# Optimization experiments

Measured on AMD Instinct MI355X. Metric: run time of the kernel, lower is better.

## Reference

```python
import jax, jax.numpy as jnp
import numpy as np
import math

DIM = 1024
NUM_HEADS = 16
QUANTUM_HEADS = 2
HEAD_DIM = DIM // NUM_HEADS          # 64
TRAD_HEADS = NUM_HEADS - QUANTUM_HEADS  # 14
B, S = 1, 1024
STEPS = 2048
LN_EPS = 1e-5


def setup_inputs() -> dict:
    key = jax.random.key(0)
    ks = jax.random.split(key, 10)
    hd2 = 2 * HEAD_DIM
    return {
        "x": jax.random.normal(ks[0], (B, S, DIM), jnp.float32),
        # to_quantum_state: Linear(head_dim -> 2*head_dim) + LayerNorm + Tanh (shared across quantum heads)
        "qs_W": jax.random.normal(ks[1], (hd2, HEAD_DIM), jnp.float32) / math.sqrt(HEAD_DIM),
        "qs_b": jnp.zeros((hd2,), jnp.float32),
        "ln_g": jnp.ones((hd2,), jnp.float32),
        "ln_b": jnp.zeros((hd2,), jnp.float32),
        # per-quantum-head scalars
        "q_freq": jax.random.normal(ks[2], (QUANTUM_HEADS,), jnp.float32) * 0.02,
        "q_shift": jax.random.normal(ks[3], (QUANTUM_HEADS,), jnp.float32) * 0.02,
        # traditional head projections (no bias)
        "Wq": jax.random.normal(ks[4], (TRAD_HEADS * HEAD_DIM, DIM), jnp.float32) / math.sqrt(DIM),
        "Wk": jax.random.normal(ks[5], (TRAD_HEADS * HEAD_DIM, DIM), jnp.float32) / math.sqrt(DIM),
        "Wv": jax.random.normal(ks[6], (TRAD_HEADS * HEAD_DIM, DIM), jnp.float32) / math.sqrt(DIM),
        # output projection (with bias)
        "Wo": jax.random.normal(ks[7], (DIM, DIM), jnp.float32) / math.sqrt(DIM),
        "bo": jnp.zeros((DIM,), jnp.float32),
    }


def _layernorm(h, g, b):
    mu = jnp.mean(h, axis=-1, keepdims=True)
    var = jnp.mean(jnp.square(h - mu), axis=-1, keepdims=True)
    return (h - mu) * jax.lax.rsqrt(var + LN_EPS) * g + b


def _forward(x, qs_W, qs_b, ln_g, ln_b, q_freq, q_shift, Wq, Wk, Wv, Wo, bo):
    cos_table = jnp.cos(jnp.linspace(0.0, 2.0 * math.pi, STEPS).astype(jnp.float32))
    scale = 1.0 / math.sqrt(HEAD_DIM)
    two_pi = 2.0 * math.pi

    outs = []
    # ---- quantum heads (small fixed loop over structurally distinct heads) ----
    for h in range(QUANTUM_HEADS):
        xh = x[..., h * HEAD_DIM:(h + 1) * HEAD_DIM]          # (B,S,hd)
        qs = jnp.tanh(_layernorm(xh @ qs_W.T + qs_b, ln_g, ln_b))  # (B,S,2hd)
        amp, phase = jnp.split(qs, 2, axis=-1)                 # each (B,S,hd)
        # per (query pos i, key pos j, feature d) phase difference
        pd = (phase[:, :, None, :] - phase[:, None, :, :]) * q_freq[h] + q_shift[h]  # (B,S,S,hd)
        idx = jnp.floor(jnp.mod(pd / two_pi * STEPS, STEPS)).astype(jnp.int32)
        interf = cos_table[idx]                                # lookup-table gather, (B,S,S,hd)
        attn = jnp.einsum('bid,bjd,bijd->bij', amp, amp, interf) * scale
        attn = jax.nn.softmax(attn, axis=-1)
        outs.append(attn @ xh)                                 # (B,S,hd), values are the raw head slice

    # ---- traditional heads: standard multi-head attention ----
    q = (x @ Wq.T).reshape(B, S, TRAD_HEADS, HEAD_DIM)
    k = (x @ Wk.T).reshape(B, S, TRAD_HEADS, HEAD_DIM)
    v = (x @ Wv.T).reshape(B, S, TRAD_HEADS, HEAD_DIM)
    scores = jnp.einsum('bqhd,bkhd->bhqk', q, k) * scale       # (B,Ht,S,S)
    probs = jax.nn.softmax(scores, axis=-1)
    trad = jnp.einsum('bhqk,bkhd->bqhd', probs, v).reshape(B, S, TRAD_HEADS * HEAD_DIM)
    outs.append(trad)

    out = jnp.concatenate(outs, axis=-1)                       # (B,S,DIM)
    return out @ Wo.T + bo


def reference(x, qs_W, qs_b, ln_g, ln_b, q_freq, q_shift, Wq, Wk, Wv, Wo, bo):
    return _forward(x, qs_W, qs_b, ln_g, ln_b, q_freq, q_shift, Wq, Wk, Wv, Wo, bo)
```

## Files before the change

kernel.cpp:

```cpp
#include <hip/hip_runtime.h>
#include <hip/hip_bf16.h>
#include <math.h>

#define DIMX 1024
#define SEQ  1024
#define HD   64
#define QH   2
#define TH   14
#define QKVN 2688
#define LN_EPS 1e-5f
#define NB_F2B 4736
#define NB_QPREP 1024
#define NB_XT 32

typedef __bf16 bf16x8 __attribute__((ext_vector_type(8)));
typedef float  f32x4  __attribute__((ext_vector_type(4)));
typedef unsigned short u16x8 __attribute__((ext_vector_type(8)));

__device__ inline unsigned short f2b_rne(float f) {
  unsigned int u = __float_as_uint(f);
  unsigned int r = (u + 0x7FFF + ((u >> 16) & 1)) >> 16;
  return (unsigned short)r;
}

__device__ inline float waveRedSum(float v) {
  #pragma unroll
  for (int off = 32; off; off >>= 1) v += __shfl_xor(v, off, 64);
  return v;
}

__global__ __launch_bounds__(256) void k_prep(
    const float* __restrict__ x, const float* __restrict__ qsW,
    const float* __restrict__ qsb, const float* __restrict__ lng,
    const float* __restrict__ lnb, const float* __restrict__ qfreq,
    const float* __restrict__ qshift,
    const float* __restrict__ wq, const float* __restrict__ wk,
    const float* __restrict__ wv, const float* __restrict__ wo,
    unsigned short* __restrict__ x_bf, unsigned short* __restrict__ wqkv_bf,
    unsigned short* __restrict__ wo_bf,
    unsigned short* __restrict__ qcs, unsigned short* __restrict__ kcs,
    unsigned short* __restrict__ xt) {
  __shared__ float xrow2[2][HD];
  __shared__ float redm[2][2], redv[2][2];
  __shared__ float qsv2[2][128];
  __shared__ unsigned short ttile[64][72];
  int t = threadIdx.x;
  int bid = blockIdx.x;
  if (bid < NB_F2B) {
    long i = ((long)bid * 256 + t) * 4;
    float4 v;
    unsigned short* dst;
    if (i < 1048576) {
      v = *reinterpret_cast<const float4*>(x + i);
      dst = x_bf + i;
    } else if (i < 3801088) {
      long j = i - 1048576;
      const float* s = (j < 917504) ? wq + j
                     : (j < 1835008) ? wk + (j - 917504)
                                     : wv + (j - 1835008);
      v = *reinterpret_cast<const float4*>(s);
      dst = wqkv_bf + j;
    } else {
      long j = i - 3801088;
      v = *reinterpret_cast<const float4*>(wo + j);
      dst = wo_bf + j;
    }
    ushort4 o;
    o.x = f2b_rne(v.x); o.y = f2b_rne(v.y); o.z = f2b_rne(v.z); o.w = f2b_rne(v.w);
    *reinterpret_cast<ushort4*>(dst) = o;
  } else if (bid < NB_F2B + NB_QPREP) {
    int half = t >> 7, o = t & 127;
    int row = (bid - NB_F2B) * 2 + half;
    int h = row >> 10, i = row & 1023;
    if (o < HD) xrow2[half][o] = x[i * DIMX + h * HD + o];
    __syncthreads();
    float s = qsb[o];
    #pragma unroll
    for (int d = 0; d < HD; d += 4) {
      float4 w = *reinterpret_cast<const float4*>(qsW + o * HD + d);
      float4 xv = *reinterpret_cast<const float4*>(&xrow2[half][d]);
      s += xv.x * w.x + xv.y * w.y + xv.z * w.z + xv.w * w.w;
    }
    int wid = (o >> 6), lane = o & 63;
    float ws = waveRedSum(s);
    if (lane == 0) redm[half][wid] = ws;
    __syncthreads();
    float mu = (redm[half][0] + redm[half][1]) * (1.0f / 128.0f);
    float dv = s - mu;
    float ws2 = waveRedSum(dv * dv);
    if (lane == 0) redv[half][wid] = ws2;
    __syncthreads();
    float var = (redv[half][0] + redv[half][1]) * (1.0f / 128.0f);
    float y = dv * rsqrtf(var + LN_EPS) * lng[o] + lnb[o];
    qsv2[half][o] = tanhf(y);
    __syncthreads();
    float freq = qfreq[h], shift = qshift[h];
    size_t base = ((size_t)h * 1024 + i) * 128;
    if (o < HD) {
      float amp = qsv2[half][o];
      float a = qsv2[half][64 + o] * freq + shift;
      float sn, cs;
      __sincosf(a, &sn, &cs);
      qcs[base + o]      = f2b_rne(amp * cs);
      qcs[base + 64 + o] = f2b_rne(amp * sn);
    } else {
      int d = o - 64;
      float amp = qsv2[half][d];
      float bAng = qsv2[half][64 + d] * freq;
      float sn, cs;
      __sincosf(bAng, &sn, &cs);
      kcs[base + d]      = f2b_rne(amp * cs);
      kcs[base + 64 + d] = f2b_rne(amp * sn);
    }
  } else {
    int b = bid - (NB_F2B + NB_QPREP);
    int h = b >> 4, kv0 = (b & 15) * 64;
    #pragma unroll
    for (int pass = 0; pass < 2; ++pass) {
      int s = pass * 256 + t;
      int r = s >> 3, c8 = (s & 7) * 8;
      const float* src = x + (size_t)(kv0 + r) * DIMX + h * 64 + c8;
      float4 a = *reinterpret_cast<const float4*>(src);
      float4 b4 = *reinterpret_cast<const float4*>(src + 4);
      ushort4 o1, o2;
      o1.x = f2b_rne(a.x);  o1.y = f2b_rne(a.y);  o1.z = f2b_rne(a.z);  o1.w = f2b_rne(a.w);
      o2.x = f2b_rne(b4.x); o2.y = f2b_rne(b4.y); o2.z = f2b_rne(b4.z); o2.w = f2b_rne(b4.w);
      *reinterpret_cast<ushort4*>(&ttile[r][c8]) = o1;
      *reinterpret_cast<ushort4*>(&ttile[r][c8 + 4]) = o2;
    }
    __syncthreads();
    #pragma unroll
    for (int pass = 0; pass < 2; ++pass) {
      int s = pass * 256 + t;
      int d = s >> 3, k8 = (s & 7) * 8;
      u16x8 o;
      #pragma unroll
      for (int j = 0; j < 8; ++j) o[j] = ttile[k8 + j][d];
      *reinterpret_cast<u16x8*>(xt + (size_t)h * 65536 + (size_t)d * 1024 + kv0 + k8) = o;
    }
  }
}

template <int DQK, int NT>
__global__ __launch_bounds__(256) void k_fattn2(
    const unsigned short* __restrict__ Qb, long q_hstep, int ldq,
    const unsigned short* __restrict__ Kb, long k_hstep, int ldk,
    const unsigned short* __restrict__ Vtb, long v_hstep, int slot0,
    float* __restrict__ pout, float* __restrict__ pml) {
  const int LQ = DQK + 8;
  const int KREG = DQK / 32;
  __shared__ unsigned short Qs[64 * (DQK + 8)];
  __shared__ unsigned short KV0[64 * (DQK + 8)];
  __shared__ unsigned short KV1[64 * (DQK + 8)];
  __shared__ unsigned short Ps[64 * 72];
  int h = blockIdx.y, q0 = blockIdx.x * 64, split = blockIdx.z;
  int kv0 = split * (NT * 64);
  int slot = slot0 + h * gridDim.z + split;
  int t = threadIdx.x, lane = t & 63, w = t >> 6;
  int g = lane >> 4, li = lane & 15;
  const unsigned short* Qp = Qb + (size_t)h * q_hstep;
  const unsigned short* Kp = Kb + (size_t)h * k_hstep;
  const unsigned short* Vp = Vtb + (size_t)h * v_hstep;

  #pragma unroll
  for (int i = 0; i < DQK / 32; ++i) {
    int s = i * 64 + lane;
    int r = s / (DQK / 8), c8 = (s % (DQK / 8)) * 8;
    u16x8 v = *reinterpret_cast<const u16x8*>(Qp + (size_t)(q0 + w * 16 + r) * ldq + c8);
    *reinterpret_cast<u16x8*>(&Qs[(w * 16 + r) * LQ + c8]) = v;
  }

  u16x8 kreg[KREG], vreg[2];
  auto loadK = [&](int tile) {
    int j0 = kv0 + tile * 64;
    #pragma unroll
    for (int i = 0; i < KREG; ++i) {
      int s = i * 256 + t;
      int r = s / (DQK / 8), c8 = (s % (DQK / 8)) * 8;
      kreg[i] = *reinterpret_cast<const u16x8*>(Kp + (size_t)(j0 + r) * ldk + c8);
    }
  };
  auto writeK = [&](int buf) {
    unsigned short* Kd = buf ? KV1 : KV0;
    #pragma unroll
    for (int i = 0; i < KREG; ++i) {
      int s = i * 256 + t;
      int r = s / (DQK / 8), c8 = (s % (DQK / 8)) * 8;
      *reinterpret_cast<u16x8*>(&Kd[r * LQ + c8]) = kreg[i];
    }
  };
  auto loadV = [&](int tile) {
    int j0 = kv0 + tile * 64;
    #pragma unroll
    for (int i = 0; i < 2; ++i) {
      int s = i * 256 + t;
      int d = s >> 3, c8 = (s & 7) * 8;
      vreg[i] = *reinterpret_cast<const u16x8*>(Vp + (size_t)d * 1024 + j0 + c8);
    }
  };
  auto writeV = [&](int buf) {
    unsigned short* Vd = buf ? KV1 : KV0;
    #pragma unroll
    for (int i = 0; i < 2; ++i) {
      int s = i * 256 + t;
      int d = s >> 3, c8 = (s & 7) * 8;
      *reinterpret_cast<u16x8*>(&Vd[d * 72 + c8]) = vreg[i];
    }
  };

  loadK(0); writeK(0); loadK(1); loadV(0);
  __syncthreads();

  f32x4 s_all[NT][4] = {};

  #pragma unroll
  for (int tile = 0; tile < NT; ++tile) {
    const unsigned short* Ksc = (tile & 1) ? KV1 : KV0;
    if (tile < NT - 1) writeK((tile + 1) & 1);
    if (tile < NT - 2) loadK(tile + 2);
    if (tile == NT - 1) writeV(0);
    #pragma unroll
    for (int kk = 0; kk < DQK / 32; ++kk) {
      bf16x8 aq = *reinterpret_cast<const bf16x8*>(&Qs[(w * 16 + li) * LQ + kk * 32 + g * 8]);
      #pragma unroll
      for (int n = 0; n < 4; ++n) {
        bf16x8 bk = *reinterpret_cast<const bf16x8*>(&Ksc[(n * 16 + li) * LQ + kk * 32 + g * 8]);
        s_all[tile][n] = __builtin_amdgcn_mfma_f32_16x16x32_bf16(aq, bk, s_all[tile][n], 0, 0, 0);
      }
    }
    __syncthreads();
  }

  loadV(1);

  float mrow[4], lrow[4];
  #pragma unroll
  for (int r = 0; r < 4; ++r) {
    float tm = -1e30f;
    #pragma unroll
    for (int tile = 0; tile < NT; ++tile)
      #pragma unroll
      for (int n = 0; n < 4; ++n) tm = fmaxf(tm, s_all[tile][n][r]);
    #pragma unroll
    for (int m = 1; m < 16; m <<= 1) tm = fmaxf(tm, __shfl_xor(tm, m, 64));
    float rs = 0.f;
    #pragma unroll
    for (int tile = 0; tile < NT; ++tile)
      #pragma unroll
      for (int n = 0; n < 4; ++n) {
        float p = __expf((s_all[tile][n][r] - tm) * 0.125f);
        s_all[tile][n][r] = p;
        rs += p;
      }
    #pragma unroll
    for (int m = 1; m < 16; m <<= 1) rs += __shfl_xor(rs, m, 64);
    mrow[r] = tm; lrow[r] = rs;
  }

  f32x4 acc_o[4] = {};
  #pragma unroll
  for (int tile = 0; tile < NT; ++tile) {
    const unsigned short* Vsc = (tile & 1) ? KV1 : KV0;
    if (tile < NT - 1) writeV((tile + 1) & 1);
    if (tile < NT - 2) loadV(tile + 2);
    #pragma unroll
    for (int n = 0; n < 4; ++n)
      #pragma unroll
      for (int r = 0; r < 4; ++r)
        Ps[(w * 16 + g * 4 + r) * 72 + n * 16 + li] = f2b_rne(s_all[tile][n][r]);
    #pragma unroll
    for (int kk = 0; kk < 2; ++kk) {
      bf16x8 ap = *reinterpret_cast<const bf16x8*>(&Ps[(w * 16 + li) * 72 + kk * 32 + g * 8]);
      #pragma unroll
      for (int n = 0; n < 4; ++n) {
        bf16x8 bv = *reinterpret_cast<const bf16x8*>(&Vsc[(n * 16 + li) * 72 + kk * 32 + g * 8]);
        acc_o[n] = __builtin_amdgcn_mfma_f32_16x16x32_bf16(ap, bv, acc_o[n], 0, 0, 0);
      }
    }
    __syncthreads();
  }

  size_t rowbase = (size_t)slot * 1024;
  #pragma unroll
  for (int r = 0; r < 4; ++r) {
    int qr = q0 + w * 16 + g * 4 + r;
    #pragma unroll
    for (int n = 0; n < 4; ++n)
      pout[(rowbase + qr) * 64 + n * 16 + li] = acc_o[n][r];
    if (li == 0) {
      pml[(rowbase + qr) * 2 + 0] = mrow[r];
      pml[(rowbase + qr) * 2 + 1] = lrow[r];
    }
  }
}

__global__ __launch_bounds__(256) void k_fmerge(
    const float* __restrict__ pout, const float* __restrict__ pml,
    unsigned short* __restrict__ concat) {
  int rq = blockIdx.x * 4 + (threadIdx.x >> 6);
  int lh = rq >> 10, q = rq & 1023;
  int d = threadIdx.x & 63;
  int s0 = (lh < 2) ? lh * 8 : 16 + (lh - 2) * 4;
  int ns = (lh < 2) ? 8 : 4;
  float m_s[8], l_s[8];
  float M = -1e30f;
  #pragma unroll
  for (int s = 0; s < 8; ++s) {
    if (s < ns) {
      size_t rb = (size_t)(s0 + s) * 1024 + q;
      m_s[s] = pml[rb * 2 + 0];
      l_s[s] = pml[rb * 2 + 1];
      M = fmaxf(M, m_s[s]);
    }
  }
  float num = 0.f, den = 0.f;
  #pragma unroll
  for (int s = 0; s < 8; ++s) {
    if (s < ns) {
      float wgt = __expf((m_s[s] - M) * 0.125f);
      num += wgt * pout[((size_t)(s0 + s) * 1024 + q) * 64 + d];
      den += wgt * l_s[s];
    }
  }
  concat[(size_t)q * DIMX + lh * 64 + d] = f2b_rne(num / den);
}

template <int HAS_BIAS, int BF16_OUT>
__global__ __launch_bounds__(256) void k_gemm64s(
    const unsigned short* __restrict__ A, const unsigned short* __restrict__ B,
    void* __restrict__ Cv, const float* __restrict__ bias,
    unsigned short* __restrict__ vtp,
    int K, int lda, int ldb, int ldc) {
  __shared__ unsigned short As[64 * 64];
  __shared__ unsigned short Bs[64 * 64];
  int t = threadIdx.x, lane = t & 63, w = t >> 6;
  int wr = w >> 1, wc = w & 1;
  int g = lane >> 4, li = lane & 15;
  int mb = blockIdx.y * 64, nb = blockIdx.x * 64;
  int rstg = t >> 3;
  int cswz = (((t & 7) ^ (rstg & 7)) * 8);
  f32x4 acc[2][2] = {};
  for (int kb = 0; kb < K; kb += 64) {
    __syncthreads();
    #pragma unroll
    for (int i = 0; i < 2; ++i) {
      __builtin_amdgcn_global_load_lds(
          (const __attribute__((address_space(1))) unsigned int*)(A + (size_t)(mb + i * 32 + rstg) * lda + kb + cswz),
          (__attribute__((address_space(3))) unsigned int*)(As + i * 2048 + t * 8), 16, 0, 0);
      __builtin_amdgcn_global_load_lds(
          (const __attribute__((address_space(1))) unsigned int*)(B + (size_t)(nb + i * 32 + rstg) * ldb + kb + cswz),
          (__attribute__((address_space(3))) unsigned int*)(Bs + i * 2048 + t * 8), 16, 0, 0);
    }
    __syncthreads();
    #pragma unroll
    for (int kk = 0; kk < 2; ++kk) {
      bf16x8 af[2], bfr[2];
      #pragma unroll
      for (int m = 0; m < 2; ++m) {
        int r = wr * 32 + m * 16 + li;
        int cb = kk * 4 + g;
        af[m] = *reinterpret_cast<const bf16x8*>(&As[r * 64 + ((cb ^ (r & 7)) * 8)]);
      }
      #pragma unroll
      for (int n = 0; n < 2; ++n) {
        int r = wc * 32 + n * 16 + li;
        int cb = kk * 4 + g;
        bfr[n] = *reinterpret_cast<const bf16x8*>(&Bs[r * 64 + ((cb ^ (r & 7)) * 8)]);
      }
      #pragma unroll
      for (int m = 0; m < 2; ++m)
        #pragma unroll
        for (int n = 0; n < 2; ++n)
          acc[m][n] = __builtin_amdgcn_mfma_f32_16x16x32_bf16(af[m], bfr[n], acc[m][n], 0, 0, 0);
    }
  }
  if (vtp != nullptr && nb >= 1792) {
    #pragma unroll
    for (int m = 0; m < 2; ++m) {
      int row0 = mb + wr * 32 + m * 16 + g * 4;
      #pragma unroll
      for (int n = 0; n < 2; ++n) {
        int colrel = nb - 1792 + wc * 32 + n * 16 + li;
        #pragma unroll
        for (int r = 0; r < 4; ++r)
          vtp[(size_t)colrel * 1024 + row0 + r] = f2b_rne(acc[m][n][r]);
      }
    }
    return;
  }
  #pragma unroll
  for (int m = 0; m < 2; ++m) {
    int row0 = mb + wr * 32 + m * 16 + g * 4;
    #pragma unroll
    for (int n = 0; n < 2; ++n) {
      int col = nb + wc * 32 + n * 16 + li;
      float bval = HAS_BIAS ? bias[col] : 0.0f;
      #pragma unroll
      for (int r = 0; r < 4; ++r) {
        size_t idx = (size_t)(row0 + r) * ldc + col;
        if (BF16_OUT) ((unsigned short*)Cv)[idx] = f2b_rne(acc[m][n][r] + bval);
        else          ((float*)Cv)[idx] = acc[m][n][r] + bval;
      }
    }
  }
}

extern "C" void kernel_launch(void* const* d_in, const int* in_sizes, int n_in,
                              void* d_out, int out_size, void* d_ws, size_t ws_size,
                              hipStream_t stream) {
  const float* x      = (const float*)d_in[0];
  const float* qsW    = (const float*)d_in[1];
  const float* qsb    = (const float*)d_in[2];
  const float* lng    = (const float*)d_in[3];
  const float* lnb    = (const float*)d_in[4];
  const float* qfreq  = (const float*)d_in[5];
  const float* qshift = (const float*)d_in[6];
  const float* Wq     = (const float*)d_in[7];
  const float* Wk     = (const float*)d_in[8];
  const float* Wv     = (const float*)d_in[9];
  const float* Wo     = (const float*)d_in[10];
  const float* bo     = (const float*)d_in[11];
  float* out = (float*)d_out;

  char* ws = (char*)d_ws;
  size_t off = 0;
  auto alloc = [&](size_t bytes) { char* p = ws + off; off += (bytes + 255) & ~(size_t)255; return p; };
  unsigned short* x_bf      = (unsigned short*)alloc((size_t)SEQ * DIMX * 2);
  unsigned short* wqkv_bf   = (unsigned short*)alloc((size_t)QKVN * DIMX * 2);
  unsigned short* wo_bf     = (unsigned short*)alloc((size_t)DIMX * DIMX * 2);
  unsigned short* concat_bf = (unsigned short*)alloc((size_t)SEQ * DIMX * 2);
  unsigned short* qkv_bf    = (unsigned short*)alloc((size_t)SEQ * QKVN * 2);
  unsigned short* qcs       = (unsigned short*)alloc((size_t)QH * SEQ * 128 * 2);
  unsigned short* kcs       = (unsigned short*)alloc((size_t)QH * SEQ * 128 * 2);
  unsigned short* vt        = (unsigned short*)alloc((size_t)TH * HD * SEQ * 2);
  unsigned short* xt        = (unsigned short*)alloc((size_t)QH * HD * SEQ * 2);
  float*          pout      = (float*)alloc((size_t)72 * SEQ * 64 * 4);
  float*          pml       = (float*)alloc((size_t)72 * SEQ * 2 * 4);

  k_prep<<<NB_F2B + NB_QPREP + NB_XT, 256, 0, stream>>>(
      x, qsW, qsb, lng, lnb, qfreq, qshift, Wq, Wk, Wv, Wo,
      x_bf, wqkv_bf, wo_bf, qcs, kcs, xt);

  k_gemm64s<0, 1><<<dim3(QKVN / 64, SEQ / 64), 256, 0, stream>>>(
      x_bf, wqkv_bf, qkv_bf, nullptr, vt, DIMX, DIMX, DIMX, QKVN);

  k_fattn2<64, 4><<<dim3(16, TH, 4), 256, 0, stream>>>(
      qkv_bf, 64, QKVN, qkv_bf + 896, 64, QKVN, vt, (long)HD * SEQ, 16, pout, pml);
  k_fattn2<128, 2><<<dim3(16, QH, 8), 256, 0, stream>>>(
      qcs, (long)SEQ * 128, 128, kcs, (long)SEQ * 128, 128, xt, (long)HD * SEQ, 0, pout, pml);

  k_fmerge<<<16 * SEQ / 4, 256, 0, stream>>>(pout, pml, concat_bf);

  k_gemm64s<1, 0><<<dim3(DIMX / 64, SEQ / 64), 256, 0, stream>>>(
      concat_bf, wo_bf, out, bo, nullptr, DIMX, DIMX, DIMX, DIMX);
}
```

Baseline: 79.63 us.

## Co-schedule quantum attention with QKV GEMM in one launch, widen GEMM K-tile

Merges the quantum-head attention blocks and the QKV projection GEMM into a single kernel that picks its role from the block index, so the two independent stages run concurrently and one launch is saved. The GEMM now stages K-tiles of 128 instead of 64, halving the loop-iteration and barrier count. It also adds XCD-aware block-index swizzles and keeps Q fragments in registers instead of LDS. In exchange, the fused kernel must reserve the larger shared-memory footprint for every block, which can lower occupancy for the GEMM blocks.

```diff
diff --git a/kernel.cpp b/kernel.cpp
--- a/kernel.cpp
+++ b/kernel.cpp
@@ -142,33 +142,26 @@
 }
 
 template <int DQK, int NT>
-__global__ __launch_bounds__(256) void k_fattn2(
-    const unsigned short* __restrict__ Qb, long q_hstep, int ldq,
-    const unsigned short* __restrict__ Kb, long k_hstep, int ldk,
-    const unsigned short* __restrict__ Vtb, long v_hstep, int slot0,
+__device__ __forceinline__ void dev_fattn2(
+    char* smem,
+    const unsigned short* __restrict__ Qp, int ldq,
+    const unsigned short* __restrict__ Kp, int ldk,
+    const unsigned short* __restrict__ Vp,
+    int q0, int kv0, int slot,
     float* __restrict__ pout, float* __restrict__ pml) {
   const int LQ = DQK + 8;
   const int KREG = DQK / 32;
-  __shared__ unsigned short Qs[64 * (DQK + 8)];
-  __shared__ unsigned short KV0[64 * (DQK + 8)];
-  __shared__ unsigned short KV1[64 * (DQK + 8)];
-  __shared__ unsigned short Ps[64 * 72];
-  int h = blockIdx.y, q0 = blockIdx.x * 64, split = blockIdx.z;
-  int kv0 = split * (NT * 64);
-  int slot = slot0 + h * gridDim.z + split;
+  unsigned short* KV0 = (unsigned short*)smem;
+  unsigned short* KV1 = KV0 + 64 * LQ;
+  unsigned short* Ps  = KV1 + 64 * LQ;
   int t = threadIdx.x, lane = t & 63, w = t >> 6;
   int g = lane >> 4, li = lane & 15;
-  const unsigned short* Qp = Qb + (size_t)h * q_hstep;
-  const unsigned short* Kp = Kb + (size_t)h * k_hstep;
-  const unsigned short* Vp = Vtb + (size_t)h * v_hstep;
-
-  #pragma unroll
-  for (int i = 0; i < DQK / 32; ++i) {
-    int s = i * 64 + lane;
-    int r = s / (DQK / 8), c8 = (s % (DQK / 8)) * 8;
-    u16x8 v = *reinterpret_cast<const u16x8*>(Qp + (size_t)(q0 + w * 16 + r) * ldq + c8);
-    *reinterpret_cast<u16x8*>(&Qs[(w * 16 + r) * LQ + c8]) = v;
-  }
+
+  bf16x8 aq[KREG];
+  #pragma unroll
+  for (int kk = 0; kk < KREG; ++kk)
+    aq[kk] = *reinterpret_cast<const bf16x8*>(
+        Qp + (size_t)(q0 + w * 16 + li) * ldq + kk * 32 + g * 8);
 
   u16x8 kreg[KREG], vreg[2];
   auto loadK = [&](int tile) {
@@ -208,7 +201,9 @@
     }
   };
 
-  loadK(0); writeK(0); loadK(1); loadV(0);
+  loadK(0); writeK(0);
+  if (NT > 1) loadK(1);
+  loadV(0);
   __syncthreads();
 
   f32x4 s_all[NT][4] = {};
@@ -220,18 +215,17 @@
     if (tile < NT - 2) loadK(tile + 2);
     if (tile == NT - 1) writeV(0);
     #pragma unroll
-    for (int kk = 0; kk < DQK / 32; ++kk) {
-      bf16x8 aq = *reinterpret_cast<const bf16x8*>(&Qs[(w * 16 + li) * LQ + kk * 32 + g * 8]);
+    for (int kk = 0; kk < KREG; ++kk) {
       #pragma unroll
       for (int n = 0; n < 4; ++n) {
         bf16x8 bk = *reinterpret_cast<const bf16x8*>(&Ksc[(n * 16 + li) * LQ + kk * 32 + g * 8]);
-        s_all[tile][n] = __builtin_amdgcn_mfma_f32_16x16x32_bf16(aq, bk, s_all[tile][n], 0, 0, 0);
-      }
-    }
-    __syncthreads();
-  }
-
-  loadV(1);
+        s_all[tile][n] = __builtin_amdgcn_mfma_f32_16x16x32_bf16(aq[kk], bk, s_all[tile][n], 0, 0, 0);
+      }
+    }
+    __syncthreads();
+  }
+
+  if (NT > 1) loadV(1);
 
   float mrow[4], lrow[4];
   #pragma unroll
@@ -292,6 +286,125 @@
       pml[(rowbase + qr) * 2 + 1] = lrow[r];
     }
   }
+}
+
+template <int HAS_BIAS, int BF16_OUT>
+__device__ __forceinline__ void dev_gemm64(
+    char* smem,
+    const unsigned short* __restrict__ A, const unsigned short* __restrict__ B,
+    void* __restrict__ Cv, const float* __restrict__ bias,
+    unsigned short* __restrict__ vtp,
+    int bx, int by, int K, int lda, int ldb, int ldc) {
+  unsigned short* As = (unsigned short*)smem;
+  unsigned short* Bs = As + 64 * 128;
+  int t = threadIdx.x, lane = t & 63, w = t >> 6;
+  int wr = w >> 1, wc = w & 1;
+  int g = lane >> 4, li = lane & 15;
+  int mb = by * 64, nb = bx * 64;
+  int rstg = t >> 4;
+  int cs = t & 15;
+  f32x4 acc[2][2] = {};
+  for (int kb = 0; kb < K; kb += 128) {
+    __syncthreads();
+    #pragma unroll
+    for (int i = 0; i < 4; ++i) {
+      int row = i * 16 + rstg;
+      int csw = ((cs ^ (row & 7)) * 8);
+      __builtin_amdgcn_global_load_lds(
+          (const __attribute__((address_space(1))) unsigned int*)(A + (size_t)(mb + row) * lda + kb + csw),
+          (__attribute__((address_space(3))) unsigned int*)(As + row * 128 + cs * 8), 16, 0, 0);
+      __builtin_amdgcn_global_load_lds(
+          (const __attribute__((address_space(1))) unsigned int*)(B + (size_t)(nb + row) * ldb + kb + csw),
+          (__attribute__((address_space(3))) unsigned int*)(Bs + row * 128 + cs * 8), 16, 0, 0);
+    }
+    __syncthreads();
+    #pragma unroll
+    for (int kk = 0; kk < 4; ++kk) {
+      bf16x8 af[2], bfr[2];
+      #pragma unroll
+      for (int m = 0; m < 2; ++m) {
+        int r = wr * 32 + m * 16 + li;
+        int cb = kk * 4 + g;
+        af[m] = *reinterpret_cast<const bf16x8*>(&As[r * 128 + ((cb ^ (r & 7)) * 8)]);
+      }
+      #pragma unroll
+      for (int n = 0; n < 2; ++n) {
+        int r = wc * 32 + n * 16 + li;
+        int cb = kk * 4 + g;
+        bfr[n] = *reinterpret_cast<const bf16x8*>(&Bs[r * 128 + ((cb ^ (r & 7)) * 8)]);
+      }
+      #pragma unroll
+      for (int m = 0; m < 2; ++m)
+        #pragma unroll
+        for (int n = 0; n < 2; ++n)
+          acc[m][n] = __builtin_amdgcn_mfma_f32_16x16x32_bf16(af[m], bfr[n], acc[m][n], 0, 0, 0);
+    }
+  }
+  if (vtp != nullptr && nb >= 1792) {
+    #pragma unroll
+    for (int m = 0; m < 2; ++m) {
+      int row0 = mb + wr * 32 + m * 16 + g * 4;
+      #pragma unroll
+      for (int n = 0; n < 2; ++n) {
+        int colrel = nb - 1792 + wc * 32 + n * 16 + li;
+        #pragma unroll
+        for (int r = 0; r < 4; ++r)
+          vtp[(size_t)colrel * 1024 + row0 + r] = f2b_rne(acc[m][n][r]);
+      }
+    }
+    return;
+  }
+  #pragma unroll
+  for (int m = 0; m < 2; ++m) {
+    int row0 = mb + wr * 32 + m * 16 + g * 4;
+    #pragma unroll
+    for (int n = 0; n < 2; ++n) {
+      int col = nb + wc * 32 + n * 16 + li;
+      float bval = HAS_BIAS ? bias[col] : 0.0f;
+      #pragma unroll
+      for (int r = 0; r < 4; ++r) {
+        size_t idx = (size_t)(row0 + r) * ldc + col;
+        if (BF16_OUT) ((unsigned short*)Cv)[idx] = f2b_rne(acc[m][n][r] + bval);
+        else          ((float*)Cv)[idx] = acc[m][n][r] + bval;
+      }
+    }
+  }
+}
+
+__global__ __launch_bounds__(256) void k_qkvq(
+    const unsigned short* __restrict__ x_bf, const unsigned short* __restrict__ wqkv,
+    unsigned short* __restrict__ qkv, unsigned short* __restrict__ vt,
+    const unsigned short* __restrict__ qcs, const unsigned short* __restrict__ kcs,
+    const unsigned short* __restrict__ xt,
+    float* __restrict__ pout, float* __restrict__ pml) {
+  __shared__ __align__(16) char smem[44032];
+  int bid = blockIdx.x;
+  if (bid < 256) {
+    int qt = bid & 15, h = (bid >> 4) & 1, split = bid >> 5;
+    dev_fattn2<128, 2>(smem, qcs + (size_t)h * SEQ * 128, 128,
+                       kcs + (size_t)h * SEQ * 128, 128,
+                       xt + (size_t)h * 65536,
+                       qt * 64, split * 128, h * 8 + split, pout, pml);
+  } else {
+    int gb = bid - 256;
+    int swz = (gb & 7) * 84 + (gb >> 3);
+    int by = swz / 42, bx = swz % 42;
+    dev_gemm64<0, 1>(smem, x_bf, wqkv, qkv, nullptr, vt, bx, by, DIMX, DIMX, DIMX, QKVN);
+  }
+}
+
+__global__ __launch_bounds__(256) void k_tattn(
+    const unsigned short* __restrict__ qkv, const unsigned short* __restrict__ vt,
+    float* __restrict__ pout, float* __restrict__ pml) {
+  __shared__ __align__(16) char smem[27648];
+  int bid = blockIdx.x;
+  int swz = (bid & 7) * 112 + (bid >> 3);
+  int qt = swz & 15, hs = swz >> 4;
+  int h = hs % 14, split = hs / 14;
+  dev_fattn2<64, 4>(smem, qkv + h * 64, QKVN,
+                    qkv + 896 + h * 64, QKVN,
+                    vt + (size_t)h * 65536,
+                    qt * 64, split * 256, 16 + h * 4 + split, pout, pml);
 }
 
 __global__ __launch_bounds__(256) void k_fmerge(
@@ -325,84 +438,14 @@
   concat[(size_t)q * DIMX + lh * 64 + d] = f2b_rne(num / den);
 }
 
-template <int HAS_BIAS, int BF16_OUT>
-__global__ __launch_bounds__(256) void k_gemm64s(
-    const unsigned short* __restrict__ A, const unsigned short* __restrict__ B,
-    void* __restrict__ Cv, const float* __restrict__ bias,
-    unsigned short* __restrict__ vtp,
-    int K, int lda, int ldb, int ldc) {
-  __shared__ unsigned short As[64 * 64];
-  __shared__ unsigned short Bs[64 * 64];
-  int t = threadIdx.x, lane = t & 63, w = t >> 6;
-  int wr = w >> 1, wc = w & 1;
-  int g = lane >> 4, li = lane & 15;
-  int mb = blockIdx.y * 64, nb = blockIdx.x * 64;
-  int rstg = t >> 3;
-  int cswz = (((t & 7) ^ (rstg & 7)) * 8);
-  f32x4 acc[2][2] = {};
-  for (int kb = 0; kb < K; kb += 64) {
-    __syncthreads();
-    #pragma unroll
-    for (int i = 0; i < 2; ++i) {
-      __builtin_amdgcn_global_load_lds(
-          (const __attribute__((address_space(1))) unsigned int*)(A + (size_t)(mb + i * 32 + rstg) * lda + kb + cswz),
-          (__attribute__((address_space(3))) unsigned int*)(As + i * 2048 + t * 8), 16, 0, 0);
-      __builtin_amdgcn_global_load_lds(
-          (const __attribute__((address_space(1))) unsigned int*)(B + (size_t)(nb + i * 32 + rstg) * ldb + kb + cswz),
-          (__attribute__((address_space(3))) unsigned int*)(Bs + i * 2048 + t * 8), 16, 0, 0);
-    }
-    __syncthreads();
-    #pragma unroll
-    for (int kk = 0; kk < 2; ++kk) {
-      bf16x8 af[2], bfr[2];
-      #pragma unroll
-      for (int m = 0; m < 2; ++m) {
-        int r = wr * 32 + m * 16 + li;
-        int cb = kk * 4 + g;
-        af[m] = *reinterpret_cast<const bf16x8*>(&As[r * 64 + ((cb ^ (r & 7)) * 8)]);
-      }
-      #pragma unroll
-      for (int n = 0; n < 2; ++n) {
-        int r = wc * 32 + n * 16 + li;
-        int cb = kk * 4 + g;
-        bfr[n] = *reinterpret_cast<const bf16x8*>(&Bs[r * 64 + ((cb ^ (r & 7)) * 8)]);
-      }
-      #pragma unroll
-      for (int m = 0; m < 2; ++m)
-        #pragma unroll
-        for (int n = 0; n < 2; ++n)
-          acc[m][n] = __builtin_amdgcn_mfma_f32_16x16x32_bf16(af[m], bfr[n], acc[m][n], 0, 0, 0);
-    }
-  }
-  if (vtp != nullptr && nb >= 1792) {
-    #pragma unroll
-    for (int m = 0; m < 2; ++m) {
-      int row0 = mb + wr * 32 + m * 16 + g * 4;
-      #pragma unroll
-      for (int n = 0; n < 2; ++n) {
-        int colrel = nb - 1792 + wc * 32 + n * 16 + li;
-        #pragma unroll
-        for (int r = 0; r < 4; ++r)
-          vtp[(size_t)colrel * 1024 + row0 + r] = f2b_rne(acc[m][n][r]);
-      }
-    }
-    return;
-  }
-  #pragma unroll
-  for (int m = 0; m < 2; ++m) {
-    int row0 = mb + wr * 32 + m * 16 + g * 4;
-    #pragma unroll
-    for (int n = 0; n < 2; ++n) {
-      int col = nb + wc * 32 + n * 16 + li;
-      float bval = HAS_BIAS ? bias[col] : 0.0f;
-      #pragma unroll
-      for (int r = 0; r < 4; ++r) {
-        size_t idx = (size_t)(row0 + r) * ldc + col;
-        if (BF16_OUT) ((unsigned short*)Cv)[idx] = f2b_rne(acc[m][n][r] + bval);
-        else          ((float*)Cv)[idx] = acc[m][n][r] + bval;
-      }
-    }
-  }
+__global__ __launch_bounds__(256) void k_oproj(
+    const unsigned short* __restrict__ concat, const unsigned short* __restrict__ wo_bf,
+    float* __restrict__ out, const float* __restrict__ bo) {
+  __shared__ __align__(16) char smem[32768];
+  int bid = blockIdx.x;
+  int swz = (bid & 7) * 32 + (bid >> 3);
+  int by = swz / 16, bx = swz % 16;
+  dev_gemm64<1, 0>(smem, concat, wo_bf, out, bo, nullptr, bx, by, DIMX, DIMX, DIMX, DIMX);
 }
 
 extern "C" void kernel_launch(void* const* d_in, const int* in_sizes, int n_in,
@@ -441,16 +484,11 @@
       x, qsW, qsb, lng, lnb, qfreq, qshift, Wq, Wk, Wv, Wo,
       x_bf, wqkv_bf, wo_bf, qcs, kcs, xt);
 
-  k_gemm64s<0, 1><<<dim3(QKVN / 64, SEQ / 64), 256, 0, stream>>>(
-      x_bf, wqkv_bf, qkv_bf, nullptr, vt, DIMX, DIMX, DIMX, QKVN);
-
-  k_fattn2<64, 4><<<dim3(16, TH, 4), 256, 0, stream>>>(
-      qkv_bf, 64, QKVN, qkv_bf + 896, 64, QKVN, vt, (long)HD * SEQ, 16, pout, pml);
-  k_fattn2<128, 2><<<dim3(16, QH, 8), 256, 0, stream>>>(
-      qcs, (long)SEQ * 128, 128, kcs, (long)SEQ * 128, 128, xt, (long)HD * SEQ, 0, pout, pml);
+  k_qkvq<<<928, 256, 0, stream>>>(x_bf, wqkv_bf, qkv_bf, vt, qcs, kcs, xt, pout, pml);
+
+  k_tattn<<<896, 256, 0, stream>>>(qkv_bf, vt, pout, pml);
 
   k_fmerge<<<16 * SEQ / 4, 256, 0, stream>>>(pout, pml, concat_bf);
 
-  k_gemm64s<1, 0><<<dim3(DIMX / 64, SEQ / 64), 256, 0, stream>>>(
-      concat_bf, wo_bf, out, bo, nullptr, DIMX, DIMX, DIMX, DIMX);
-}
+  k_oproj<<<256, 256, 0, stream>>>(concat_bf, wo_bf, out, bo);
+}
```

New measurement: 77.66 us. 1.03x faster.
